# Optimization experiments

Hardware: AMD Instinct MI355X
Metric: run time of the kernel (lower is better)

## Reference

```python
import jax, jax.numpy as jnp
import numpy as np

B, TE, TD, D, U = 8, 256, 256, 256, 256


def setup_inputs() -> dict:
    key = jax.random.key(0)
    k1, k2, k3, k4, k5 = jax.random.split(key, 5)
    glorot = lambda k, shape: jax.random.uniform(
        k, shape, jnp.float32,
        -np.sqrt(6.0 / (shape[0] + shape[1])), np.sqrt(6.0 / (shape[0] + shape[1])))
    return {
        "en_seq": jax.random.normal(k1, (B, TE, D), jnp.float32),
        "de_seq": jax.random.normal(k2, (B, TD, D), jnp.float32),
        "w_en": glorot(k3, (D, U)),
        "w_de": glorot(k4, (D, U)),
        "nu": glorot(k5, (U, 1)),
    }


def reference(en_seq, de_seq, w_en, w_de, nu):
    # Additive co-attention scores.
    ae = jnp.einsum('bte,eu->btu', en_seq, w_en)          # (B, Te, U)
    ad = jnp.einsum('bsd,du->bsu', de_seq, w_de)          # (B, Td, U)
    # co_m[b, td, te, u] = ae[b, te, u] + ad[b, td, u]  (matches K.repeat / repeat_elements layout)
    co = jnp.tanh(ad[:, :, None, :] + ae[:, None, :, :])  # (B, Td, Te, U)
    mu = jnp.einsum('bstu,ul->bst', co, nu)               # (B, Td, Te)
    alphas = jax.nn.softmax(mu, axis=-1)                  # softmax over en time
    max_mu = jnp.max(mu, axis=-1)                         # (B, Td)
    max_alphas = jax.nn.softmax(max_mu, axis=-1)          # softmax over de time
    h_hat = jnp.sum(de_seq * max_alphas[..., None], axis=1)  # (B, Dd)
    sum_en = jnp.einsum('bst,bte->bse', alphas, en_seq)      # (B, Td, De)
    output = jnp.concatenate(
        [de_seq, sum_en, de_seq * sum_en, de_seq * h_hat[:, None, :]], axis=-1)
    return output  # (B, Td, 4*D)
```

## Files before the change

kernel.cpp:

```cpp
#include <hip/hip_runtime.h>

#define B_   8
#define TE_  256
#define TD_  256
#define D_   256
#define U_   256

#define EET_OFF   0
#define ED_OFF    524288
#define MAXMU_OFF 1048576

__device__ __forceinline__ float fexp2(float x) {
#if __has_builtin(__builtin_amdgcn_exp2f)
  return __builtin_amdgcn_exp2f(x);
#else
  return exp2f(x);
#endif
}
__device__ __forceinline__ float frcp(float x) {
#if __has_builtin(__builtin_amdgcn_rcpf)
  return __builtin_amdgcn_rcpf(x);
#else
  return 1.0f / x;
#endif
}

#define LOG2E_F 1.4426950408889634f
#define TWO_LOG2E_F 2.8853900817779268f

__global__ __launch_bounds__(512) void coatt_k1_proj(
    const float* __restrict__ en, const float* __restrict__ de,
    const float* __restrict__ w_en, const float* __restrict__ w_de,
    float* __restrict__ ws) {
  const int which = blockIdx.z;
  const float* __restrict__ A = which ? de : en;
  const float* __restrict__ W = which ? w_de : w_en;
  const int rowBase = blockIdx.y * 64;
  const int colBase = blockIdx.x * 64;
  __shared__ float smem[2][2][32][68];
  const int tid = threadIdx.x;
  const int tx = tid & 31, ty = tid >> 5;
  const int aRow = tid >> 3, aC4 = tid & 7;
  const int bK = tid >> 4, bC4 = tid & 15;

  float4 aR = *(const float4*)&A[(size_t)(rowBase + aRow) * D_ + aC4 * 4];
  float4 bR = *(const float4*)&W[(size_t)bK * U_ + colBase + bC4 * 4];
  {
    float v[4]; *(float4*)v = aR;
#pragma unroll
    for (int j = 0; j < 4; ++j) smem[0][0][aC4 * 4 + j][aRow] = v[j];
    *(float4*)&smem[1][0][bK][bC4 * 4] = bR;
  }
  __syncthreads();

  float acc[4][2] = {};
#define K1_COMPUTE(BUF)                                              \
  _Pragma("unroll")                                                  \
  for (int k = 0; k < 32; ++k) {                                     \
    float av[4], bv[2];                                              \
    *(float4*)av = *(const float4*)&smem[0][BUF][k][ty * 4];         \
    *(float2*)bv = *(const float2*)&smem[1][BUF][k][tx * 2];         \
    _Pragma("unroll")                                                \
    for (int i = 0; i < 4; ++i)                                      \
      _Pragma("unroll")                                              \
      for (int j = 0; j < 2; ++j)                                    \
        acc[i][j] = fmaf(av[i], bv[j], acc[i][j]);                   \
  }

  for (int kc = 0; kc < 7; ++kc) {
    const int k0 = (kc + 1) * 32;
    aR = *(const float4*)&A[(size_t)(rowBase + aRow) * D_ + k0 + aC4 * 4];
    bR = *(const float4*)&W[(size_t)(k0 + bK) * U_ + colBase + bC4 * 4];
    const int cur = kc & 1, nxt = cur ^ 1;
    K1_COMPUTE(cur)
    {
      float v[4]; *(float4*)v = aR;
#pragma unroll
      for (int j = 0; j < 4; ++j) smem[0][nxt][aC4 * 4 + j][aRow] = v[j];
      *(float4*)&smem[1][nxt][bK][bC4 * 4] = bR;
    }
    __syncthreads();
  }
  K1_COMPUTE(1)

  if (which) {
    float* __restrict__ outp = ws + ED_OFF;
#pragma unroll
    for (int i = 0; i < 4; ++i) {
      float2 o;
      o.x = fexp2(acc[i][0] * TWO_LOG2E_F);
      o.y = fexp2(acc[i][1] * TWO_LOG2E_F);
      *(float2*)&outp[(size_t)(rowBase + ty * 4 + i) * U_ + colBase + tx * 2] = o;
    }
  } else {
    __syncthreads();
    float* Cs = &smem[0][0][0][0];
#pragma unroll
    for (int i = 0; i < 4; ++i)
#pragma unroll
      for (int j = 0; j < 2; ++j)
        Cs[(tx * 2 + j) * 69 + ty * 4 + i] = fexp2(acc[i][j] * TWO_LOG2E_F);
    __syncthreads();
    float* __restrict__ outp = ws + EET_OFF;
    const int b = rowBase >> 8, t0 = rowBase & 255;
    const int u4Base = colBase >> 2;
#pragma unroll
    for (int kk = 0; kk < 2; ++kk) {
      const int q = tid + 512 * kk;
      const int u4l = q >> 6, tl = q & 63;
      float4 v;
      v.x = Cs[(u4l * 4 + 0) * 69 + tl];
      v.y = Cs[(u4l * 4 + 1) * 69 + tl];
      v.z = Cs[(u4l * 4 + 2) * 69 + tl];
      v.w = Cs[(u4l * 4 + 3) * 69 + tl];
      *(float4*)&outp[(size_t)((b * 64 + u4Base + u4l) * 256 + t0 + tl) * 4] = v;
    }
  }
}

__global__ __launch_bounds__(256) void coatt_k24(
    const float* __restrict__ en, const float* __restrict__ de,
    const float* __restrict__ nu, float* __restrict__ ws,
    float* __restrict__ out) {
  const float* __restrict__ EeT = ws + EET_OFF;
  const float* __restrict__ Ed = ws + ED_OFF;
  float* __restrict__ maxmu = ws + MAXMU_OFF;
  const int b = blockIdx.y;
  const int sBase = blockIdx.x * 4;
  const int tid = threadIdx.x;
  const int w = tid >> 6, lane = tid & 63;
  const float* __restrict__ Ee_b = EeT + (size_t)b * U_ * TE_ + tid * 4;
  const float* __restrict__ Ed_b = Ed + (size_t)(b * TD_ + sBase) * U_;

  float acc0 = 0.f, acc1 = 0.f, acc2 = 0.f, acc3 = 0.f;
#pragma unroll 4
  for (int u4 = 0; u4 < 64; ++u4) {
    const float4 nv = *(const float4*)&nu[u4 * 4];
    const float4 e0 = *(const float4*)&Ed_b[0 * U_ + u4 * 4];
    const float4 e1 = *(const float4*)&Ed_b[1 * U_ + u4 * 4];
    const float4 e2 = *(const float4*)&Ed_b[2 * U_ + u4 * 4];
    const float4 e3 = *(const float4*)&Ed_b[3 * U_ + u4 * 4];
    const float4 ee4 = *(const float4*)&Ee_b[u4 * 1024];
    const float* nvp = (const float*)&nv;
    const float* eep = (const float*)&ee4;
    const float* p0 = (const float*)&e0;
    const float* p1 = (const float*)&e1;
    const float* p2 = (const float*)&e2;
    const float* p3 = (const float*)&e3;
#pragma unroll
    for (int j = 0; j < 4; ++j) {
      acc0 = fmaf(nvp[j], frcp(fmaf(p0[j], eep[j], 1.0f)), acc0);
      acc1 = fmaf(nvp[j], frcp(fmaf(p1[j], eep[j], 1.0f)), acc1);
      acc2 = fmaf(nvp[j], frcp(fmaf(p2[j], eep[j], 1.0f)), acc2);
      acc3 = fmaf(nvp[j], frcp(fmaf(p3[j], eep[j], 1.0f)), acc3);
    }
  }
  float v[4] = {-2.f * acc0, -2.f * acc1, -2.f * acc2, -2.f * acc3};
  __shared__ float part[4][4];
  __shared__ float als[4][256];
  float m[4];
#pragma unroll
  for (int s = 0; s < 4; ++s) {
    m[s] = v[s];
#pragma unroll
    for (int off = 32; off > 0; off >>= 1) m[s] = fmaxf(m[s], __shfl_xor(m[s], off));
    if (lane == 0) part[s][w] = m[s];
  }
  __syncthreads();
#pragma unroll
  for (int s = 0; s < 4; ++s)
    m[s] = fmaxf(fmaxf(part[s][0], part[s][1]), fmaxf(part[s][2], part[s][3]));
  __syncthreads();
  float e[4], sm[4];
#pragma unroll
  for (int s = 0; s < 4; ++s) {
    e[s] = fexp2((v[s] - m[s]) * LOG2E_F);
    sm[s] = e[s];
#pragma unroll
    for (int off = 32; off > 0; off >>= 1) sm[s] += __shfl_xor(sm[s], off);
    if (lane == 0) part[s][w] = sm[s];
  }
  __syncthreads();
#pragma unroll
  for (int s = 0; s < 4; ++s) {
    const float tot = (part[s][0] + part[s][1]) + (part[s][2] + part[s][3]);
    als[s][tid] = e[s] * frcp(tot);
  }
  if (tid == 0) {
#pragma unroll
    for (int s = 0; s < 4; ++s) maxmu[b * TD_ + sBase + s] = m[s];
  }
  __syncthreads();

  const int d = tid;
  const float* __restrict__ en_b = en + (size_t)b * TE_ * D_ + d;
  float sa0 = 0.f, sa1 = 0.f, sa2 = 0.f, sa3 = 0.f;
#pragma unroll 4
  for (int t4 = 0; t4 < 64; ++t4) {
    const float4 a0 = *(const float4*)&als[0][t4 * 4];
    const float4 a1 = *(const float4*)&als[1][t4 * 4];
    const float4 a2 = *(const float4*)&als[2][t4 * 4];
    const float4 a3 = *(const float4*)&als[3][t4 * 4];
    float env[4];
#pragma unroll
    for (int j = 0; j < 4; ++j) env[j] = en_b[(t4 * 4 + j) * D_];
    const float* q0 = (const float*)&a0;
    const float* q1 = (const float*)&a1;
    const float* q2 = (const float*)&a2;
    const float* q3 = (const float*)&a3;
#pragma unroll
    for (int j = 0; j < 4; ++j) {
      sa0 = fmaf(q0[j], env[j], sa0);
      sa1 = fmaf(q1[j], env[j], sa1);
      sa2 = fmaf(q2[j], env[j], sa2);
      sa3 = fmaf(q3[j], env[j], sa3);
    }
  }
  const float se[4] = {sa0, sa1, sa2, sa3};
#pragma unroll
  for (int s = 0; s < 4; ++s) {
    const float dd = de[(size_t)(b * TD_ + sBase + s) * D_ + d];
    float* o = out + (size_t)(b * TD_ + sBase + s) * (4 * D_);
    o[d] = dd;
    o[D_ + d] = se[s];
    o[2 * D_ + d] = dd * se[s];
  }
}

__global__ __launch_bounds__(256) void coatt_k3_hhat(
    const float* __restrict__ de, const float* __restrict__ ws,
    float* __restrict__ out) {
  const float* __restrict__ maxmu = ws + MAXMU_OFF;
  const int b = blockIdx.y;
  const int dBase = blockIdx.x * 32;
  const int tid = threadIdx.x;
  const int w = tid >> 6, lane = tid & 63;
  __shared__ float red[8];
  __shared__ float malpha[256];
  __shared__ float acc_red[256];
  __shared__ float hh_s[32];
  const float vv = maxmu[b * TD_ + tid];
  float m = vv;
#pragma unroll
  for (int off = 32; off > 0; off >>= 1) m = fmaxf(m, __shfl_xor(m, off));
  if (lane == 0) red[w] = m;
  __syncthreads();
  m = fmaxf(fmaxf(red[0], red[1]), fmaxf(red[2], red[3]));
  const float e = fexp2((vv - m) * LOG2E_F);
  float sm = e;
#pragma unroll
  for (int off = 32; off > 0; off >>= 1) sm += __shfl_xor(sm, off);
  if (lane == 0) red[4 + w] = sm;
  __syncthreads();
  sm = (red[4] + red[5]) + (red[6] + red[7]);
  malpha[tid] = e * frcp(sm);
  __syncthreads();
  const int dl = tid & 31, sg = tid >> 5;
  float acc = 0.f;
  for (int s = sg * 32; s < sg * 32 + 32; ++s)
    acc = fmaf(de[(size_t)(b * TD_ + s) * D_ + dBase + dl], malpha[s], acc);
  acc_red[tid] = acc;
  __syncthreads();
  if (tid < 32) {
    float t = acc_red[tid];
#pragma unroll
    for (int g = 1; g < 8; ++g) t += acc_red[g * 32 + tid];
    hh_s[tid] = t;
  }
  __syncthreads();
  const float hh = hh_s[dl];
#pragma unroll 4
  for (int s = sg; s < TD_; s += 8) {
    const float dd = de[(size_t)(b * TD_ + s) * D_ + dBase + dl];
    out[(size_t)(b * TD_ + s) * (4 * D_) + 3 * D_ + dBase + dl] = dd * hh;
  }
}

extern "C" void kernel_launch(void* const* d_in, const int* in_sizes, int n_in,
                              void* d_out, int out_size, void* d_ws, size_t ws_size,
                              hipStream_t stream) {
  (void)in_sizes; (void)n_in; (void)out_size; (void)ws_size;
  const float* en   = (const float*)d_in[0];
  const float* de   = (const float*)d_in[1];
  const float* w_en = (const float*)d_in[2];
  const float* w_de = (const float*)d_in[3];
  const float* nu   = (const float*)d_in[4];
  float* out = (float*)d_out;
  float* ws  = (float*)d_ws;

  coatt_k1_proj<<<dim3(4, 32, 2), 512, 0, stream>>>(en, de, w_en, w_de, ws);
  coatt_k24<<<dim3(64, 8), 256, 0, stream>>>(en, de, nu, ws, out);
  coatt_k3_hhat<<<dim3(8, 8), 256, 0, stream>>>(de, ws, out);
}
```

Measured before the change: 114.4 us.

## Rebalance projection tiles and split score kernel across two half-blocks

The projection kernel now uses 256 threads, each computing a 4x4 output tile instead of 4x2, and loads two float4s per thread per stage. The main score/softmax kernel doubles its block to 512 threads, with each half handling two decoder rows, and stages Ed and nu in shared memory. The weighted sum over encoder time is split across the halves and combined through shared memory. Grid indexing interleaves batches so neighbouring blocks spread across batch. This raises per-block parallelism for the transcendental-heavy inner loop at the cost of more shared memory and an extra sync/reduction.

```diff
diff --git a/kernel.cpp b/kernel.cpp
--- a/kernel.cpp
+++ b/kernel.cpp
@@ -28,7 +28,7 @@
 #define LOG2E_F 1.4426950408889634f
 #define TWO_LOG2E_F 2.8853900817779268f
 
-__global__ __launch_bounds__(512) void coatt_k1_proj(
+__global__ __launch_bounds__(256) void coatt_k1_proj(
     const float* __restrict__ en, const float* __restrict__ de,
     const float* __restrict__ w_en, const float* __restrict__ w_de,
     float* __restrict__ ws) {
@@ -37,47 +37,56 @@
   const float* __restrict__ W = which ? w_de : w_en;
   const int rowBase = blockIdx.y * 64;
   const int colBase = blockIdx.x * 64;
-  __shared__ float smem[2][2][32][68];
+  __shared__ float smem[2][2][32][69];
   const int tid = threadIdx.x;
-  const int tx = tid & 31, ty = tid >> 5;
-  const int aRow = tid >> 3, aC4 = tid & 7;
-  const int bK = tid >> 4, bC4 = tid & 15;
-
-  float4 aR = *(const float4*)&A[(size_t)(rowBase + aRow) * D_ + aC4 * 4];
-  float4 bR = *(const float4*)&W[(size_t)bK * U_ + colBase + bC4 * 4];
-  {
-    float v[4]; *(float4*)v = aR;
-#pragma unroll
-    for (int j = 0; j < 4; ++j) smem[0][0][aC4 * 4 + j][aRow] = v[j];
-    *(float4*)&smem[1][0][bK][bC4 * 4] = bR;
-  }
-  __syncthreads();
-
-  float acc[4][2] = {};
+  const int tx = tid & 15, ty = tid >> 4;
+  const int aRow0 = tid >> 3, aC4 = tid & 7;
+  const int bK0 = tid >> 4, bC4 = tid & 15;
+  float4 aR[2], bR[2];
+
+#pragma unroll
+  for (int kk = 0; kk < 2; ++kk) {
+    aR[kk] = *(const float4*)&A[(size_t)(rowBase + aRow0 + 32 * kk) * D_ + aC4 * 4];
+    bR[kk] = *(const float4*)&W[(size_t)(bK0 + 16 * kk) * U_ + colBase + bC4 * 4];
+  }
+#pragma unroll
+  for (int kk = 0; kk < 2; ++kk) {
+    float v[4]; *(float4*)v = aR[kk];
+#pragma unroll
+    for (int j = 0; j < 4; ++j) smem[0][0][aC4 * 4 + j][aRow0 + 32 * kk] = v[j];
+    *(float4*)&smem[1][0][bK0 + 16 * kk][bC4 * 4] = bR[kk];
+  }
+  __syncthreads();
+
+  float acc[4][4] = {};
 #define K1_COMPUTE(BUF)                                              \
   _Pragma("unroll")                                                  \
   for (int k = 0; k < 32; ++k) {                                     \
-    float av[4], bv[2];                                              \
+    float av[4], bv[4];                                              \
     *(float4*)av = *(const float4*)&smem[0][BUF][k][ty * 4];         \
-    *(float2*)bv = *(const float2*)&smem[1][BUF][k][tx * 2];         \
+    *(float4*)bv = *(const float4*)&smem[1][BUF][k][tx * 4];         \
     _Pragma("unroll")                                                \
     for (int i = 0; i < 4; ++i)                                      \
       _Pragma("unroll")                                              \
-      for (int j = 0; j < 2; ++j)                                    \
+      for (int j = 0; j < 4; ++j)                                    \
         acc[i][j] = fmaf(av[i], bv[j], acc[i][j]);                   \
   }
 
   for (int kc = 0; kc < 7; ++kc) {
     const int k0 = (kc + 1) * 32;
-    aR = *(const float4*)&A[(size_t)(rowBase + aRow) * D_ + k0 + aC4 * 4];
-    bR = *(const float4*)&W[(size_t)(k0 + bK) * U_ + colBase + bC4 * 4];
+#pragma unroll
+    for (int kk = 0; kk < 2; ++kk) {
+      aR[kk] = *(const float4*)&A[(size_t)(rowBase + aRow0 + 32 * kk) * D_ + k0 + aC4 * 4];
+      bR[kk] = *(const float4*)&W[(size_t)(k0 + bK0 + 16 * kk) * U_ + colBase + bC4 * 4];
+    }
     const int cur = kc & 1, nxt = cur ^ 1;
     K1_COMPUTE(cur)
-    {
-      float v[4]; *(float4*)v = aR;
-#pragma unroll
-      for (int j = 0; j < 4; ++j) smem[0][nxt][aC4 * 4 + j][aRow] = v[j];
-      *(float4*)&smem[1][nxt][bK][bC4 * 4] = bR;
+#pragma unroll
+    for (int kk = 0; kk < 2; ++kk) {
+      float v[4]; *(float4*)v = aR[kk];
+#pragma unroll
+      for (int j = 0; j < 4; ++j) smem[0][nxt][aC4 * 4 + j][aRow0 + 32 * kk] = v[j];
+      *(float4*)&smem[1][nxt][bK0 + 16 * kk][bC4 * 4] = bR[kk];
     }
     __syncthreads();
   }
@@ -87,10 +96,12 @@
     float* __restrict__ outp = ws + ED_OFF;
 #pragma unroll
     for (int i = 0; i < 4; ++i) {
-      float2 o;
+      float4 o;
       o.x = fexp2(acc[i][0] * TWO_LOG2E_F);
       o.y = fexp2(acc[i][1] * TWO_LOG2E_F);
-      *(float2*)&outp[(size_t)(rowBase + ty * 4 + i) * U_ + colBase + tx * 2] = o;
+      o.z = fexp2(acc[i][2] * TWO_LOG2E_F);
+      o.w = fexp2(acc[i][3] * TWO_LOG2E_F);
+      *(float4*)&outp[(size_t)(rowBase + ty * 4 + i) * U_ + colBase + tx * 4] = o;
     }
   } else {
     __syncthreads();
@@ -98,15 +109,15 @@
 #pragma unroll
     for (int i = 0; i < 4; ++i)
 #pragma unroll
-      for (int j = 0; j < 2; ++j)
-        Cs[(tx * 2 + j) * 69 + ty * 4 + i] = fexp2(acc[i][j] * TWO_LOG2E_F);
+      for (int j = 0; j < 4; ++j)
+        Cs[(tx * 4 + j) * 69 + ty * 4 + i] = fexp2(acc[i][j] * TWO_LOG2E_F);
     __syncthreads();
     float* __restrict__ outp = ws + EET_OFF;
     const int b = rowBase >> 8, t0 = rowBase & 255;
     const int u4Base = colBase >> 2;
 #pragma unroll
-    for (int kk = 0; kk < 2; ++kk) {
-      const int q = tid + 512 * kk;
+    for (int kk = 0; kk < 4; ++kk) {
+      const int q = tid + 256 * kk;
       const int u4l = q >> 6, tl = q & 63;
       float4 v;
       v.x = Cs[(u4l * 4 + 0) * 69 + tl];
@@ -118,92 +129,109 @@
   }
 }
 
-__global__ __launch_bounds__(256) void coatt_k24(
+__global__ __launch_bounds__(512) void coatt_k24(
     const float* __restrict__ en, const float* __restrict__ de,
     const float* __restrict__ nu, float* __restrict__ ws,
     float* __restrict__ out) {
   const float* __restrict__ EeT = ws + EET_OFF;
   const float* __restrict__ Ed = ws + ED_OFF;
   float* __restrict__ maxmu = ws + MAXMU_OFF;
-  const int b = blockIdx.y;
-  const int sBase = blockIdx.x * 4;
+  const int id = blockIdx.x;
+  const int b = id & 7;
+  const int sBase = (id >> 3) * 4;
   const int tid = threadIdx.x;
+  const int t = tid & 255;
+  const int half = tid >> 8;
   const int w = tid >> 6, lane = tid & 63;
-  const float* __restrict__ Ee_b = EeT + (size_t)b * U_ * TE_ + tid * 4;
-  const float* __restrict__ Ed_b = Ed + (size_t)(b * TD_ + sBase) * U_;
-
-  float acc0 = 0.f, acc1 = 0.f, acc2 = 0.f, acc3 = 0.f;
+
+  __shared__ float eds[4][256];
+  __shared__ float nus[256];
+  __shared__ float als[4][256];
+  __shared__ float tp[2][4][256];
+  __shared__ float part[2][8];
+
+  {
+    const float2* src = (const float2*)(Ed + (size_t)(b * TD_ + sBase) * U_);
+    ((float2*)&eds[0][0])[tid] = src[tid];
+    if (tid < 128) ((float2*)nus)[tid] = ((const float2*)nu)[tid];
+  }
+  __syncthreads();
+
+  const float* __restrict__ Ee_b = EeT + (size_t)b * (U_ * TE_) + t * 4;
+  const int s0 = half * 2;
+  float accA0 = 0.f, accB0 = 0.f, accA1 = 0.f, accB1 = 0.f;
 #pragma unroll 4
   for (int u4 = 0; u4 < 64; ++u4) {
-    const float4 nv = *(const float4*)&nu[u4 * 4];
-    const float4 e0 = *(const float4*)&Ed_b[0 * U_ + u4 * 4];
-    const float4 e1 = *(const float4*)&Ed_b[1 * U_ + u4 * 4];
-    const float4 e2 = *(const float4*)&Ed_b[2 * U_ + u4 * 4];
-    const float4 e3 = *(const float4*)&Ed_b[3 * U_ + u4 * 4];
     const float4 ee4 = *(const float4*)&Ee_b[u4 * 1024];
+    const float4 nv = *(const float4*)&nus[u4 * 4];
+    const float4 d0 = *(const float4*)&eds[s0][u4 * 4];
+    const float4 d1 = *(const float4*)&eds[s0 + 1][u4 * 4];
+    const float* eep = (const float*)&ee4;
     const float* nvp = (const float*)&nv;
-    const float* eep = (const float*)&ee4;
-    const float* p0 = (const float*)&e0;
-    const float* p1 = (const float*)&e1;
-    const float* p2 = (const float*)&e2;
-    const float* p3 = (const float*)&e3;
+    const float* p0 = (const float*)&d0;
+    const float* p1 = (const float*)&d1;
 #pragma unroll
     for (int j = 0; j < 4; ++j) {
-      acc0 = fmaf(nvp[j], frcp(fmaf(p0[j], eep[j], 1.0f)), acc0);
-      acc1 = fmaf(nvp[j], frcp(fmaf(p1[j], eep[j], 1.0f)), acc1);
-      acc2 = fmaf(nvp[j], frcp(fmaf(p2[j], eep[j], 1.0f)), acc2);
-      acc3 = fmaf(nvp[j], frcp(fmaf(p3[j], eep[j], 1.0f)), acc3);
-    }
-  }
-  float v[4] = {-2.f * acc0, -2.f * acc1, -2.f * acc2, -2.f * acc3};
-  __shared__ float part[4][4];
-  __shared__ float als[4][256];
-  float m[4];
-#pragma unroll
-  for (int s = 0; s < 4; ++s) {
-    m[s] = v[s];
-#pragma unroll
-    for (int off = 32; off > 0; off >>= 1) m[s] = fmaxf(m[s], __shfl_xor(m[s], off));
-    if (lane == 0) part[s][w] = m[s];
-  }
-  __syncthreads();
-#pragma unroll
-  for (int s = 0; s < 4; ++s)
-    m[s] = fmaxf(fmaxf(part[s][0], part[s][1]), fmaxf(part[s][2], part[s][3]));
-  __syncthreads();
-  float e[4], sm[4];
-#pragma unroll
-  for (int s = 0; s < 4; ++s) {
-    e[s] = fexp2((v[s] - m[s]) * LOG2E_F);
-    sm[s] = e[s];
-#pragma unroll
-    for (int off = 32; off > 0; off >>= 1) sm[s] += __shfl_xor(sm[s], off);
-    if (lane == 0) part[s][w] = sm[s];
-  }
-  __syncthreads();
-#pragma unroll
-  for (int s = 0; s < 4; ++s) {
-    const float tot = (part[s][0] + part[s][1]) + (part[s][2] + part[s][3]);
-    als[s][tid] = e[s] * frcp(tot);
-  }
-  if (tid == 0) {
-#pragma unroll
-    for (int s = 0; s < 4; ++s) maxmu[b * TD_ + sBase + s] = m[s];
-  }
-  __syncthreads();
-
-  const int d = tid;
+      const float r0 = frcp(fmaf(p0[j], eep[j], 1.0f));
+      const float r1 = frcp(fmaf(p1[j], eep[j], 1.0f));
+      if (j & 1) {
+        accB0 = fmaf(nvp[j], r0, accB0);
+        accB1 = fmaf(nvp[j], r1, accB1);
+      } else {
+        accA0 = fmaf(nvp[j], r0, accA0);
+        accA1 = fmaf(nvp[j], r1, accA1);
+      }
+    }
+  }
+  float v0 = -2.f * (accA0 + accB0);
+  float v1 = -2.f * (accA1 + accB1);
+
+  float m0 = v0, m1 = v1;
+#pragma unroll
+  for (int off = 32; off > 0; off >>= 1) {
+    m0 = fmaxf(m0, __shfl_xor(m0, off));
+    m1 = fmaxf(m1, __shfl_xor(m1, off));
+  }
+  if (lane == 0) { part[0][w] = m0; part[1][w] = m1; }
+  __syncthreads();
+  const int wb = half * 4;
+  m0 = fmaxf(fmaxf(part[0][wb], part[0][wb + 1]), fmaxf(part[0][wb + 2], part[0][wb + 3]));
+  m1 = fmaxf(fmaxf(part[1][wb], part[1][wb + 1]), fmaxf(part[1][wb + 2], part[1][wb + 3]));
+  __syncthreads();
+  const float e0 = fexp2((v0 - m0) * LOG2E_F);
+  const float e1 = fexp2((v1 - m1) * LOG2E_F);
+  float sm0 = e0, sm1 = e1;
+#pragma unroll
+  for (int off = 32; off > 0; off >>= 1) {
+    sm0 += __shfl_xor(sm0, off);
+    sm1 += __shfl_xor(sm1, off);
+  }
+  if (lane == 0) { part[0][w] = sm0; part[1][w] = sm1; }
+  __syncthreads();
+  const float tot0 = (part[0][wb] + part[0][wb + 1]) + (part[0][wb + 2] + part[0][wb + 3]);
+  const float tot1 = (part[1][wb] + part[1][wb + 1]) + (part[1][wb + 2] + part[1][wb + 3]);
+  als[s0][t] = e0 * frcp(tot0);
+  als[s0 + 1][t] = e1 * frcp(tot1);
+  if (t == 0) {
+    maxmu[b * TD_ + sBase + s0] = m0;
+    maxmu[b * TD_ + sBase + s0 + 1] = m1;
+  }
+  __syncthreads();
+
+  const int d = t;
+  const int tBeg = half * 128;
   const float* __restrict__ en_b = en + (size_t)b * TE_ * D_ + d;
   float sa0 = 0.f, sa1 = 0.f, sa2 = 0.f, sa3 = 0.f;
 #pragma unroll 4
-  for (int t4 = 0; t4 < 64; ++t4) {
-    const float4 a0 = *(const float4*)&als[0][t4 * 4];
-    const float4 a1 = *(const float4*)&als[1][t4 * 4];
-    const float4 a2 = *(const float4*)&als[2][t4 * 4];
-    const float4 a3 = *(const float4*)&als[3][t4 * 4];
+  for (int t4 = 0; t4 < 32; ++t4) {
+    const int tt = tBeg + t4 * 4;
+    const float4 a0 = *(const float4*)&als[0][tt];
+    const float4 a1 = *(const float4*)&als[1][tt];
+    const float4 a2 = *(const float4*)&als[2][tt];
+    const float4 a3 = *(const float4*)&als[3][tt];
     float env[4];
 #pragma unroll
-    for (int j = 0; j < 4; ++j) env[j] = en_b[(t4 * 4 + j) * D_];
+    for (int j = 0; j < 4; ++j) env[j] = en_b[(size_t)(tt + j) * D_];
     const float* q0 = (const float*)&a0;
     const float* q1 = (const float*)&a1;
     const float* q2 = (const float*)&a2;
@@ -216,14 +244,21 @@
       sa3 = fmaf(q3[j], env[j], sa3);
     }
   }
-  const float se[4] = {sa0, sa1, sa2, sa3};
-#pragma unroll
-  for (int s = 0; s < 4; ++s) {
-    const float dd = de[(size_t)(b * TD_ + sBase + s) * D_ + d];
-    float* o = out + (size_t)(b * TD_ + sBase + s) * (4 * D_);
+  tp[half][0][d] = sa0;
+  tp[half][1][d] = sa1;
+  tp[half][2][d] = sa2;
+  tp[half][3][d] = sa3;
+  __syncthreads();
+#pragma unroll
+  for (int k = 0; k < 2; ++k) {
+    const int sl = s0 + k;
+    const float se = tp[0][sl][d] + tp[1][sl][d];
+    const int s = sBase + sl;
+    const float dd = de[(size_t)(b * TD_ + s) * D_ + d];
+    float* o = out + (size_t)(b * TD_ + s) * (4 * D_);
     o[d] = dd;
-    o[D_ + d] = se[s];
-    o[2 * D_ + d] = dd * se[s];
+    o[D_ + d] = se;
+    o[2 * D_ + d] = dd * se;
   }
 }
 
@@ -262,10 +297,10 @@
   acc_red[tid] = acc;
   __syncthreads();
   if (tid < 32) {
-    float t = acc_red[tid];
-#pragma unroll
-    for (int g = 1; g < 8; ++g) t += acc_red[g * 32 + tid];
-    hh_s[tid] = t;
+    float tsum = acc_red[tid];
+#pragma unroll
+    for (int g = 1; g < 8; ++g) tsum += acc_red[g * 32 + tid];
+    hh_s[tid] = tsum;
   }
   __syncthreads();
   const float hh = hh_s[dl];
@@ -288,7 +323,7 @@
   float* out = (float*)d_out;
   float* ws  = (float*)d_ws;
 
-  coatt_k1_proj<<<dim3(4, 32, 2), 512, 0, stream>>>(en, de, w_en, w_de, ws);
-  coatt_k24<<<dim3(64, 8), 256, 0, stream>>>(en, de, nu, ws, out);
+  coatt_k1_proj<<<dim3(4, 32, 2), 256, 0, stream>>>(en, de, w_en, w_de, ws);
+  coatt_k24<<<dim3(512), 512, 0, stream>>>(en, de, nu, ws, out);
   coatt_k3_hhat<<<dim3(8, 8), 256, 0, stream>>>(de, ws, out);
 }
```

After: 112.7 us. Within noise of the previous version (-1.5%).
